# Kernel tuning notes

Measured on AMD Instinct MI355X. Metric: run time of the kernel, lower is better.

## Reference

```python
import jax, jax.numpy as jnp
import numpy as np
from jax import lax

B, S, H, V, J, K = 8, 512, 768, 35004, 30, 9
PAD = 0

def setup_inputs() -> dict:
    key = jax.random.key(0)
    ks = jax.random.split(key, 12)
    std = 0.02
    return {
        'x': jax.random.randint(ks[0], (B, S), 0, V),
        'decoder_input': jax.random.normal(ks[1], (B, J, H), jnp.float32),
        'encoder_output': jax.random.normal(ks[2], (B, S, H), jnp.float32),
        'hidden': jax.random.normal(ks[3], (1, B, H), jnp.float32),
        'teacher': jax.random.randint(ks[4], (B, J, K), 0, V),
        'max_len': K,
        'embed': jax.random.normal(ks[5], (V, H), jnp.float32) * std,
        'w_ih': jax.random.normal(ks[6], (3 * H, H), jnp.float32) * std,
        'w_hh': jax.random.normal(ks[7], (3 * H, H), jnp.float32) * std,
        'b_ih': jnp.zeros((3 * H,), jnp.float32),
        'b_hh': jnp.zeros((3 * H,), jnp.float32),
        'wg_w': jax.random.normal(ks[8], (1, 3 * H), jnp.float32) * std,
        'wg_b': jnp.zeros((1,), jnp.float32),
    }

def gru_cell(w, h, w_ih, w_hh, b_ih, b_hh):
    # PyTorch GRU gate order: reset, update, new
    gi = w @ w_ih.T + b_ih          # [B,3H]
    gh = h @ w_hh.T + b_hh          # [B,3H]
    ir, iz, inn = jnp.split(gi, 3, axis=-1)
    hr, hz, hn = jnp.split(gh, 3, axis=-1)
    r = jax.nn.sigmoid(ir + hr)
    z = jax.nn.sigmoid(iz + hz)
    n = jnp.tanh(inn + r * hn)
    return (1.0 - z) * n + z * h

def reference(x, decoder_input, encoder_output, hidden, teacher, max_len,
              embed, w_ih, w_hh, b_ih, b_hh, wg_w, wg_b):
    mask = (x == PAD)                      # [B,S]
    batch_ix = jnp.arange(x.shape[0])[:, None]

    def tok_step(carry, teach_t):
        w, h = carry                       # w,h: [B,H]; teach_t: [B]
        h = gru_cell(w, h, w_ih, w_hh, b_ih, b_hh)
        logits_hist = jnp.einsum('bsh,bh->bs', encoder_output, h)
        logits_hist = jnp.where(mask, -1e9, logits_hist)
        a_hist = jax.nn.softmax(logits_hist, axis=-1)          # [B,S]
        a_vocab = jax.nn.softmax(h @ embed.T, axis=-1)         # [B,V]
        context = jnp.einsum('bs,bsh->bh', a_hist, encoder_output)
        p_gen = jax.nn.sigmoid(
            jnp.concatenate([w, h, context], axis=-1) @ wg_w.T + wg_b)  # [B,1]
        p_ctx = jnp.zeros_like(a_vocab).at[batch_ix, x].add(a_hist)     # scatter_add pointer copy
        p_final = p_gen * a_vocab + (1.0 - p_gen) * p_ctx
        w_next = embed[teach_t]            # teacher forcing (dropout omitted: eval mode)
        return (w_next, h), p_final

    def slot_step(h, slot_in):
        w0, teach_j = slot_in              # w0: [B,H]; teach_j: [K,B]
        (_, h), p = lax.scan(tok_step, (w0, h), teach_j)
        return h, p                        # p: [K,B,V]

    h0 = hidden[0]                                      # [B,H]
    slots = jnp.swapaxes(decoder_input, 0, 1)           # [J,B,H]
    teach = jnp.transpose(teacher, (1, 2, 0))           # [J,K,B]
    _, outs = lax.scan(slot_step, h0, (slots, teach))   # [J,K,B,V]
    return jnp.transpose(outs, (2, 0, 1, 3))            # [B,J,K,V]
```

## Files before the change

### kernel.cpp

```cpp
#include <hip/hip_runtime.h>
#include <hip/hip_bf16.h>

typedef _Float16 f16;
typedef _Float16 f16x8 __attribute__((ext_vector_type(8)));
typedef _Float16 f16x4v __attribute__((ext_vector_type(4)));
typedef _Float16 h2 __attribute__((ext_vector_type(2)));
typedef float f32x4 __attribute__((ext_vector_type(4)));
typedef unsigned ui4v __attribute__((ext_vector_type(4)));
typedef unsigned long long ull;

#define B_ 8
#define S_ 512
#define H_ 768
#define V_ 35004
#define J_ 30
#define K_ 9
#define R_ 2160
#define H3 2304
#define VMT 17
#define VNT 274


__global__ void k_zero(int* p, int n) {
    int i = blockIdx.x * 256 + threadIdx.x;
    if (i < n) p[i] = 0;
}

__global__ void k_cast(const float* __restrict__ s, f16* __restrict__ d, long n) {
    for (long i = (long)blockIdx.x * 256 + threadIdx.x; i < n; i += (long)gridDim.x * 256)
        d[i] = (f16)s[i];
}

__global__ void k_build_wall(const float* __restrict__ emb, const float* __restrict__ dec,
                             const int* __restrict__ teacher, f16* __restrict__ Wall) {
    int r = blockIdx.x;
    int b = r / 270, s = r % 270, j = s / 9, t = s % 9;
    const float* src = (t == 0) ? dec + ((long)b * J_ + j) * H_
                                : emb + (long)teacher[((long)b * J_ + j) * K_ + (t - 1)] * H_;
    f16* dst = Wall + (long)r * H_;
    for (int c = threadIdx.x; c < H_; c += 256) dst[c] = (f16)src[c];
}

__global__ void k_init_h(const float* __restrict__ hidden, ull* __restrict__ hbuf) {
    int i = blockIdx.x * 256 + threadIdx.x;
    if (i < B_ * H_) {
        int b = i / H_, u = i % H_;
        hbuf[(long)b * 1536 + u] = (ull)__float_as_uint(hidden[i]);
    }
}

typedef const __attribute__((address_space(1))) unsigned GASU;
typedef __attribute__((address_space(3))) unsigned LASU;
__device__ __forceinline__ void gld16(const f16* g, f16* l) {
    __builtin_amdgcn_global_load_lds((GASU*)g, (LASU*)l, 16, 0, 0);
}

template <int MODE>
__global__ __launch_bounds__(256) void k_gemm(const f16* __restrict__ A, const f16* __restrict__ Bm,
                                              float* __restrict__ C, const float* __restrict__ bias,
                                              int M, int N, int K, long sA, long sB, long sC) {
    A += (long)blockIdx.z * sA;
    Bm += (long)blockIdx.z * sB;
    C += (long)blockIdx.z * sC;
    const int m0 = blockIdx.y * 128, n0 = blockIdx.x * 128;
    __shared__ f16 As[128 * 32];
    __shared__ f16 Bs[128 * 32];
    const int tid = threadIdx.x, lane = tid & 63, wave = tid >> 6;
    const int wm = wave >> 1, wn = wave & 1;
    const int fr = lane & 15, kg = lane >> 4;
    f32x4 acc[4][4] = {};
    const int idxu = wave * 128;
    const int i0 = idxu + lane, i1 = idxu + 64 + lane;
    const int r0 = i0 >> 2, k80 = i0 & 3;
    const int r1 = i1 >> 2, k81 = i1 & 3;
    int ga0 = m0 + r0; if (ga0 >= M) ga0 = M - 1;
    int ga1 = m0 + r1; if (ga1 >= M) ga1 = M - 1;
    int gb0 = n0 + r0; if (gb0 >= N) gb0 = N - 1;
    int gb1 = n0 + r1; if (gb1 >= N) gb1 = N - 1;
    const f16* pa0 = A + (long)ga0 * K + k80 * 8;
    const f16* pa1 = A + (long)ga1 * K + k81 * 8;
    const f16* pb0 = Bm + (long)gb0 * K + k80 * 8;
    const f16* pb1 = Bm + (long)gb1 * K + k81 * 8;
    for (int kt = 0; kt < K; kt += 32) {
        gld16(pa0 + kt, As + idxu * 8);
        gld16(pa1 + kt, As + idxu * 8 + 512);
        gld16(pb0 + kt, Bs + idxu * 8);
        gld16(pb1 + kt, Bs + idxu * 8 + 512);
        __syncthreads();
        f16x8 af[4], bf[4];
#pragma unroll
        for (int m = 0; m < 4; ++m) af[m] = *(const f16x8*)(As + (wm * 64 + m * 16 + fr) * 32 + kg * 8);
#pragma unroll
        for (int n = 0; n < 4; ++n) bf[n] = *(const f16x8*)(Bs + (wn * 64 + n * 16 + fr) * 32 + kg * 8);
#pragma unroll
        for (int m = 0; m < 4; ++m)
#pragma unroll
            for (int n = 0; n < 4; ++n)
                acc[m][n] = __builtin_amdgcn_mfma_f32_16x16x32_f16(af[m], bf[n], acc[m][n], 0, 0, 0);
        __syncthreads();
    }
    const int crow = m0 + wm * 64 + (lane >> 4) * 4;
    const int ccol = n0 + wn * 64 + fr;
#pragma unroll
    for (int n = 0; n < 4; ++n) {
        int col = ccol + n * 16;
        if (col >= N) continue;
        float bv = (MODE == 1) ? bias[col] : 0.f;
#pragma unroll
        for (int m = 0; m < 4; ++m) {
#pragma unroll
            for (int q = 0; q < 4; ++q) {
                int row = crow + m * 16 + q;
                if (row < M) C[(long)row * N + col] = acc[m][n][q] + bv;
            }
        }
    }
}

__global__ __launch_bounds__(256) void k_attn3(const f16* __restrict__ Ahi, const f16* __restrict__ Alo,
                                               const f16* __restrict__ Bhi, const f16* __restrict__ Blo,
                                               float* __restrict__ C, int M, int N, int K,
                                               long sA, long sB, long sC) {
    const long za = (long)blockIdx.z * sA, zb = (long)blockIdx.z * sB;
    C += (long)blockIdx.z * sC;
    const int m0 = blockIdx.y * 128, n0 = blockIdx.x * 128;
    __shared__ f16 As[128 * 32];
    __shared__ f16 Bs[128 * 32];
    const int tid = threadIdx.x, lane = tid & 63, wave = tid >> 6;
    const int wm = wave >> 1, wn = wave & 1;
    const int fr = lane & 15, kg = lane >> 4;
    f32x4 acc[4][4] = {};
    const int idxu = wave * 128;
    const int i0 = idxu + lane, i1 = idxu + 64 + lane;
    const int r0 = i0 >> 2, k80 = i0 & 3;
    const int r1 = i1 >> 2, k81 = i1 & 3;
    int ga0 = m0 + r0; if (ga0 >= M) ga0 = M - 1;
    int ga1 = m0 + r1; if (ga1 >= M) ga1 = M - 1;
    int gb0 = n0 + r0; if (gb0 >= N) gb0 = N - 1;
    int gb1 = n0 + r1; if (gb1 >= N) gb1 = N - 1;
    const long oa0 = (long)ga0 * K + k80 * 8, oa1 = (long)ga1 * K + k81 * 8;
    const long ob0 = (long)gb0 * K + k80 * 8, ob1 = (long)gb1 * K + k81 * 8;
    for (int ph = 0; ph < 3; ++ph) {
        const f16* Ap = (ph == 2 ? Alo : Ahi) + za;
        const f16* Bp = (ph == 1 ? Blo : Bhi) + zb;
        for (int kt = 0; kt < K; kt += 32) {
            gld16(Ap + oa0 + kt, As + idxu * 8);
            gld16(Ap + oa1 + kt, As + idxu * 8 + 512);
            gld16(Bp + ob0 + kt, Bs + idxu * 8);
            gld16(Bp + ob1 + kt, Bs + idxu * 8 + 512);
            __syncthreads();
            f16x8 af[4], bf[4];
#pragma unroll
            for (int m = 0; m < 4; ++m) af[m] = *(const f16x8*)(As + (wm * 64 + m * 16 + fr) * 32 + kg * 8);
#pragma unroll
            for (int n = 0; n < 4; ++n) bf[n] = *(const f16x8*)(Bs + (wn * 64 + n * 16 + fr) * 32 + kg * 8);
#pragma unroll
            for (int m = 0; m < 4; ++m)
#pragma unroll
                for (int n = 0; n < 4; ++n)
                    acc[m][n] = __builtin_amdgcn_mfma_f32_16x16x32_f16(af[m], bf[n], acc[m][n], 0, 0, 0);
            __syncthreads();
        }
    }
    const int crow = m0 + wm * 64 + (lane >> 4) * 4;
    const int ccol = n0 + wn * 64 + fr;
#pragma unroll
    for (int n = 0; n < 4; ++n) {
        int col = ccol + n * 16;
        if (col >= N) continue;
#pragma unroll
        for (int m = 0; m < 4; ++m) {
#pragma unroll
            for (int q = 0; q < 4; ++q) {
                int row = crow + m * 16 + q;
                if (row < M) C[(long)row * N + col] = acc[m][n][q];
            }
        }
    }
}

__global__ __launch_bounds__(256) void k_vocab(const f16* __restrict__ A, const f16* __restrict__ Bm,
                                               float* __restrict__ C, float* __restrict__ psum) {
    const int M = R_, N = V_, K = H_;
    const int nwg = VMT * VNT;
    int lin = blockIdx.x;
    int q8 = nwg / 8, r8 = nwg % 8;
    int xcd = lin & 7, idx = lin >> 3;
    int newlin = (xcd < r8) ? xcd * (q8 + 1) + idx : r8 * (q8 + 1) + (xcd - r8) * q8 + idx;
    int mt = newlin % VMT, nt = newlin / VMT;
    const int m0 = mt * 128, n0 = nt * 128;
    __shared__ f16 As[128 * 32];
    __shared__ f16 Bs[128 * 32];
    __shared__ float rpart[2][128];
    const int tid = threadIdx.x, lane = tid & 63, wave = tid >> 6;
    const int wm = wave >> 1, wn = wave & 1;
    const int fr = lane & 15, kg = lane >> 4;
    f32x4 acc[4][4] = {};
    const int idxu = wave * 128;
    const int i0 = idxu + lane, i1 = idxu + 64 + lane;
    const int r0 = i0 >> 2, k80 = i0 & 3;
    const int r1 = i1 >> 2, k81 = i1 & 3;
    int ga0 = m0 + r0; if (ga0 >= M) ga0 = M - 1;
    int ga1 = m0 + r1; if (ga1 >= M) ga1 = M - 1;
    int gb0 = n0 + r0; if (gb0 >= N) gb0 = N - 1;
    int gb1 = n0 + r1; if (gb1 >= N) gb1 = N - 1;
    const f16* pa0 = A + (long)ga0 * K + k80 * 8;
    const f16* pa1 = A + (long)ga1 * K + k81 * 8;
    const f16* pb0 = Bm + (long)gb0 * K + k80 * 8;
    const f16* pb1 = Bm + (long)gb1 * K + k81 * 8;
    for (int kt = 0; kt < K; kt += 32) {
        gld16(pa0 + kt, As + idxu * 8);
        gld16(pa1 + kt, As + idxu * 8 + 512);
        gld16(pb0 + kt, Bs + idxu * 8);
        gld16(pb1 + kt, Bs + idxu * 8 + 512);
        __syncthreads();
        f16x8 af[4], bf[4];
#pragma unroll
        for (int m = 0; m < 4; ++m) af[m] = *(const f16x8*)(As + (wm * 64 + m * 16 + fr) * 32 + kg * 8);
#pragma unroll
        for (int n = 0; n < 4; ++n) bf[n] = *(const f16x8*)(Bs + (wn * 64 + n * 16 + fr) * 32 + kg * 8);
#pragma unroll
        for (int m = 0; m < 4; ++m)
#pragma unroll
            for (int n = 0; n < 4; ++n)
                acc[m][n] = __builtin_amdgcn_mfma_f32_16x16x32_f16(af[m], bf[n], acc[m][n], 0, 0, 0);
        __syncthreads();
    }
    const int crow = m0 + wm * 64 + (lane >> 4) * 4;
    const int ccol = n0 + wn * 64 + fr;
    float rs[4][4];
#pragma unroll
    for (int m = 0; m < 4; ++m)
#pragma unroll
        for (int q = 0; q < 4; ++q) rs[m][q] = 0.f;
#pragma unroll
    for (int n = 0; n < 4; ++n) {
        int col = ccol + n * 16;
        if (col >= N) continue;
#pragma unroll
        for (int m = 0; m < 4; ++m) {
#pragma unroll
            for (int q = 0; q < 4; ++q) {
                int row = crow + m * 16 + q;
                if (row < M) {
                    float e = __expf(acc[m][n][q]);
                    C[(long)row * N + col] = e;
                    rs[m][q] += e;
                }
            }
        }
    }
#pragma unroll
    for (int m = 0; m < 4; ++m)
#pragma unroll
        for (int q = 0; q < 4; ++q) {
            float v = rs[m][q];
            v += __shfl_xor(v, 1);
            v += __shfl_xor(v, 2);
            v += __shfl_xor(v, 4);
            v += __shfl_xor(v, 8);
            rs[m][q] = v;
        }
    if ((lane & 15) == 0) {
#pragma unroll
        for (int m = 0; m < 4; ++m)
#pragma unroll
            for (int q = 0; q < 4; ++q)
                rpart[wn][wm * 64 + (lane >> 4) * 4 + m * 16 + q] = rs[m][q];
    }
    __syncthreads();
    if (tid < 128) {
        int row = m0 + tid;
        if (row < M) psum[(long)nt * M + row] = rpart[0][tid] + rpart[1][tid];
    }
}

__device__ __forceinline__ float fd2(unsigned hv, unsigned wv, float acc) {
#if __has_builtin(__builtin_amdgcn_fdot2)
    return __builtin_amdgcn_fdot2(__builtin_bit_cast(h2, hv), __builtin_bit_cast(h2, wv), acc, false);
#else
    h2 a = __builtin_bit_cast(h2, hv), b = __builtin_bit_cast(h2, wv);
    return acc + (float)a.x * (float)b.x + (float)a.y * (float)b.y;
#endif
}

__global__ __launch_bounds__(256, 1) void k_gru(const float* __restrict__ gi,
                                                const float* __restrict__ whh,
                                                const float* __restrict__ bhh,
                                                ull* hbuf,
                                                f16* __restrict__ Hhi, f16* __restrict__ Hlo,
                                                const float* __restrict__ emb, f16* __restrict__ emb16,
                                                const float* __restrict__ enc, f16* __restrict__ ehi,
                                                f16* __restrict__ elo, f16* __restrict__ encT) {
    __shared__ ui4v wsvu[9216];
    __shared__ __align__(16) f16 hsf[768];
    __shared__ float part[2][8][32][3];
    const int tid = threadIdx.x;
    if (blockIdx.x >= 192) {
        const long pt = (long)(blockIdx.x - 192) * 256 + tid;
        const long n4 = (long)V_ * H_ / 4;
        for (long i = pt; i < n4; i += 64 * 256) {
            f32x4 v = ((const f32x4*)emb)[i];
            f16x4v r = {(f16)v.x, (f16)v.y, (f16)v.z, (f16)v.w};
            ((f16x4v*)emb16)[i] = r;
        }
        const long n4e = (long)B_ * S_ * H_ / 4;
        for (long i = pt; i < n4e; i += 64 * 256) {
            f32x4 v = ((const f32x4*)enc)[i];
            long e0 = i * 4;
            int h = (int)(e0 % H_);
            long bs = e0 / H_;
            int ss = (int)(bs % S_), bb = (int)(bs / S_);
            f16 h0 = (f16)v.x, h1 = (f16)v.y, h2v = (f16)v.z, h3 = (f16)v.w;
            f16x4v hv = {h0, h1, h2v, h3};
            ((f16x4v*)ehi)[i] = hv;
            f16x4v lv = {(f16)(v.x - (float)h0), (f16)(v.y - (float)h1),
                         (f16)(v.z - (float)h2v), (f16)(v.w - (float)h3)};
            ((f16x4v*)elo)[i] = lv;
            f16* tp = encT + ((long)bb * H_ + h) * S_ + ss;
            tp[0] = h0;
            tp[S_] = h1;
            tp[2L * S_] = h2v;
            tp[3L * S_] = h3;
        }
        return;
    }
    const int chain = blockIdx.x / 24;
    const int blk = blockIdx.x % 24;
    const int u0 = blk * 32;
    for (int idx = tid; idx < 9216; idx += 256) {
        int uu = idx & 31, k8 = (idx >> 5) % 96, g = idx / (96 * 32);
        const float* src = whh + (long)(g * H_ + u0 + uu) * H_ + k8 * 8;
        f32x4 a = *(const f32x4*)src;
        f32x4 b2 = *(const f32x4*)(src + 4);
        f16x8 pk = {(f16)a.x, (f16)a.y, (f16)a.z, (f16)a.w,
                    (f16)b2.x, (f16)b2.y, (f16)b2.z, (f16)b2.w};
        wsvu[idx] = __builtin_bit_cast(ui4v, pk);
    }
    float b_r = 0.f, b_z = 0.f, b_n = 0.f;
    if (tid < 32) {
        int c = u0 + tid;
        b_r = bhh[c];
        b_z = bhh[H_ + c];
        b_n = bhh[2 * H_ + c];
    }
    __syncthreads();
    const int u = tid & 31, q = tid >> 5, lane = tid & 63;
    const int pw = (tid >> 6) * 192 + lane;
    ui4v wreg[3][12];
#pragma unroll
    for (int g = 0; g < 3; ++g)
#pragma unroll
        for (int i = 0; i < 12; ++i)
            wreg[g][i] = wsvu[(g * 96 + q * 12 + i) * 32 + u];
    ull* base = hbuf + (long)chain * 1536;
    const bool fin = (tid < 32);
    float g0 = 0.f, g1 = 0.f, g2v = 0.f;
    if (fin) {
        const float* gp = gi + (long)chain * 270 * H3;
        int c = u0 + tid;
        g0 = gp[c];
        g1 = gp[H_ + c];
        g2v = gp[2 * H_ + c];
    }
    for (int s = 0; s < 270; ++s) {
        const ull* rb = base + (s & 1) * 768;
        ull* wb = base + ((s + 1) & 1) * 768;
        const unsigned want = (unsigned)s;
        ull v0, v1, v2, vh = 0;
        for (;;) {
            v0 = __hip_atomic_load(rb + pw, __ATOMIC_RELAXED, __HIP_MEMORY_SCOPE_AGENT);
            v1 = __hip_atomic_load(rb + pw + 64, __ATOMIC_RELAXED, __HIP_MEMORY_SCOPE_AGENT);
            v2 = __hip_atomic_load(rb + pw + 128, __ATOMIC_RELAXED, __HIP_MEMORY_SCOPE_AGENT);
            bool ok = ((unsigned)(v0 >> 32) == want) & ((unsigned)(v1 >> 32) == want) &
                      ((unsigned)(v2 >> 32) == want);
            if (fin) {
                vh = __hip_atomic_load(rb + u0 + tid, __ATOMIC_RELAXED, __HIP_MEMORY_SCOPE_AGENT);
                ok &= ((unsigned)(vh >> 32) == want);
            }
            if (ok) break;
        }
        hsf[pw] = (f16)__uint_as_float((unsigned)v0);
        hsf[pw + 64] = (f16)__uint_as_float((unsigned)v1);
        hsf[pw + 128] = (f16)__uint_as_float((unsigned)v2);
        __builtin_amdgcn_wave_barrier();
        float ar = 0.f, az = 0.f, an = 0.f;
#pragma unroll
        for (int i = 0; i < 12; ++i) {
            ui4v hv = *(const ui4v*)(&hsf[(q * 12 + i) * 8]);
            ui4v wr = wreg[0][i], wz = wreg[1][i], wn = wreg[2][i];
            ar = fd2(hv.x, wr.x, ar); ar = fd2(hv.y, wr.y, ar);
            ar = fd2(hv.z, wr.z, ar); ar = fd2(hv.w, wr.w, ar);
            az = fd2(hv.x, wz.x, az); az = fd2(hv.y, wz.y, az);
            az = fd2(hv.z, wz.z, az); az = fd2(hv.w, wz.w, az);
            an = fd2(hv.x, wn.x, an); an = fd2(hv.y, wn.y, an);
            an = fd2(hv.z, wn.z, an); an = fd2(hv.w, wn.w, an);
        }
        const int par = s & 1;
        part[par][q][u][0] = ar;
        part[par][q][u][1] = az;
        part[par][q][u][2] = an;
        __syncthreads();
        if (fin) {
            float gr = b_r, gz = b_z, gn = b_n;
#pragma unroll
            for (int qq = 0; qq < 8; ++qq) {
                gr += part[par][qq][tid][0];
                gz += part[par][qq][tid][1];
                gn += part[par][qq][tid][2];
            }
            float hold = __uint_as_float((unsigned)vh);
            float rg = 1.f / (1.f + expf(-(g0 + gr)));
            float zg = 1.f / (1.f + expf(-(g1 + gz)));
            float ng = tanhf(g2v + rg * gn);
            float hnew = (1.f - zg) * ng + zg * hold;
            int c = u0 + tid;
            ull wvv = ((ull)(unsigned)(s + 1) << 32) | (ull)__float_as_uint(hnew);
            __hip_atomic_store(wb + c, wvv, __ATOMIC_RELAXED, __HIP_MEMORY_SCOPE_AGENT);
            long row = (long)chain * 270 + s;
            f16 h16 = (f16)hnew;
            Hhi[row * H_ + c] = h16;
            Hlo[row * H_ + c] = (f16)(hnew - (float)h16);
            if (s < 269) {
                const float* gp = gi + ((long)chain * 270 + s + 1) * H3;
                g0 = gp[c];
                g1 = gp[H_ + c];
                g2v = gp[2 * H_ + c];
            }
        }
    }
}

__global__ __launch_bounds__(256) void k_attn_softmax(const float* __restrict__ lg,
                                                      const int* __restrict__ x, f16* __restrict__ ah) {
    __shared__ float red[256];
    int r = blockIdx.x, tid = threadIdx.x;
    int b = r / 270;
    const float* lr = lg + (long)r * S_;
    const int* xb = x + (long)b * S_;
    float v0 = lr[tid];
    if (xb[tid] == 0) v0 = -1e9f;
    float v1 = lr[tid + 256];
    if (xb[tid + 256] == 0) v1 = -1e9f;
    red[tid] = fmaxf(v0, v1);
    __syncthreads();
    for (int o = 128; o > 0; o >>= 1) {
        if (tid < o) red[tid] = fmaxf(red[tid], red[tid + o]);
        __syncthreads();
    }
    float m = red[0];
    __syncthreads();
    float e0 = __expf(v0 - m), e1 = __expf(v1 - m);
    red[tid] = e0 + e1;
    __syncthreads();
    for (int o = 128; o > 0; o >>= 1) {
        if (tid < o) red[tid] += red[tid + o];
        __syncthreads();
    }
    float inv = 1.f / red[0];
    ah[(long)r * S_ + tid] = (f16)(e0 * inv);
    ah[(long)r * S_ + tid + 256] = (f16)(e1 * inv);
}

__global__ __launch_bounds__(256) void k_pgen(const f16* __restrict__ Wall, const f16* __restrict__ Hhi,
                                              const f16* __restrict__ Hlo, const float* __restrict__ ctx,
                                              const float* __restrict__ wg, const float* __restrict__ wgb,
                                              float* __restrict__ pg) {
    __shared__ float red[256];
    int r = blockIdx.x, tid = threadIdx.x;
    float a = 0.f;
    for (int i = tid; i < H_; i += 256) {
        a += (float)Wall[(long)r * H_ + i] * wg[i];
        a += ((float)Hhi[(long)r * H_ + i] + (float)Hlo[(long)r * H_ + i]) * wg[H_ + i];
        a += ctx[(long)r * H_ + i] * wg[2 * H_ + i];
    }
    red[tid] = a;
    __syncthreads();
    for (int o = 128; o > 0; o >>= 1) {
        if (tid < o) red[tid] += red[tid + o];
        __syncthreads();
    }
    if (tid == 0) pg[r] = 1.f / (1.f + expf(-(red[0] + wgb[0])));
}

__global__ void k_redsum(const float* __restrict__ psum, float* __restrict__ rinv, int nb) {
    int r = blockIdx.x * 256 + threadIdx.x;
    if (r >= R_) return;
    float s = 0.f;
    for (int b = 0; b < nb; ++b) s += psum[(long)b * R_ + r];
    rinv[r] = 1.f / s;
}

__global__ __launch_bounds__(256) void k_final(float* __restrict__ out, const float* __restrict__ rinv,
                                               const float* __restrict__ pg) {
    int r = blockIdx.y;
    int i = blockIdx.x * 256 + threadIdx.x;
    if (i >= V_ / 4) return;
    float scale = pg[r] * rinv[r];
    f32x4* po = (f32x4*)(out + (long)r * V_);
    f32x4 v = po[i];
    v.x *= scale;
    v.y *= scale;
    v.z *= scale;
    v.w *= scale;
    po[i] = v;
}

__global__ __launch_bounds__(512) void k_scatter(float* __restrict__ out, const f16* __restrict__ ah,
                                                 const float* __restrict__ pg, const int* __restrict__ x) {
    int r = blockIdx.x, s = threadIdx.x;
    int b = r / 270;
    int xv = x[(long)b * S_ + s];
    if (xv == 0) return;
    float a = (float)ah[(long)r * S_ + s];
    if (a == 0.f) return;
    atomicAdd(out + (long)r * V_ + xv, (1.f - pg[r]) * a);
}

extern "C" void kernel_launch(void* const* d_in, const int* in_sizes, int n_in, void* d_out,
                              int out_size, void* d_ws, size_t ws_size, hipStream_t stream) {
    (void)in_sizes; (void)n_in; (void)out_size; (void)ws_size;
    const int* x = (const int*)d_in[0];
    const float* dec = (const float*)d_in[1];
    const float* enc = (const float*)d_in[2];
    const float* hid = (const float*)d_in[3];
    const int* tea = (const int*)d_in[4];
    const float* emb = (const float*)d_in[6];
    const float* wih = (const float*)d_in[7];
    const float* whh = (const float*)d_in[8];
    const float* bih = (const float*)d_in[9];
    const float* bhh = (const float*)d_in[10];
    const float* wgw = (const float*)d_in[11];
    const float* wgb = (const float*)d_in[12];
    float* out = (float*)d_out;

    char* w = (char*)d_ws;
    size_t off = 0;
    auto alloc = [&](size_t bytes) {
        void* p = w + off;
        off = (off + bytes + 255) & ~(size_t)255;
        return p;
    };
    ull* hbuf = (ull*)alloc(8 * 1536 * 8);
    f16* Wall = (f16*)alloc((size_t)R_ * H_ * 2);
    f16* wih16 = (f16*)alloc((size_t)H3 * H_ * 2);
    float* giA = (float*)alloc((size_t)R_ * H3 * 4);
    f16* Hhi = (f16*)alloc((size_t)R_ * H_ * 2);
    f16* Hlo = (f16*)alloc((size_t)R_ * H_ * 2);
    f16* emb16 = (f16*)alloc((size_t)V_ * H_ * 2);
    f16* ehi = (f16*)alloc((size_t)B_ * S_ * H_ * 2);
    f16* elo = (f16*)alloc((size_t)B_ * S_ * H_ * 2);
    f16* encT = (f16*)alloc((size_t)B_ * H_ * S_ * 2);
    float* lgH = (float*)alloc((size_t)R_ * S_ * 4);
    f16* ah = (f16*)alloc((size_t)R_ * S_ * 2);
    float* ctx = (float*)alloc((size_t)R_ * H_ * 4);
    float* pg = (float*)alloc(R_ * 4);
    float* psum = (float*)alloc((size_t)VNT * R_ * 4);
    float* rinv = (float*)alloc(R_ * 4);

    const int nH = 8 * 1536 * 2;
    k_zero<<<(nH + 255) / 256, 256, 0, stream>>>((int*)hbuf, nH);
    k_cast<<<512, 256, 0, stream>>>(wih, wih16, (long)H3 * H_);
    k_build_wall<<<R_, 256, 0, stream>>>(emb, dec, tea, Wall);
    k_init_h<<<24, 256, 0, stream>>>(hid, hbuf);

    {
        dim3 g(H3 / 128, (R_ + 127) / 128, 1);
        k_gemm<1><<<g, 256, 0, stream>>>(Wall, wih16, giA, bih, R_, H3, H_, 0, 0, 0);
    }
    k_gru<<<256, 256, 0, stream>>>(giA, whh, bhh, hbuf, Hhi, Hlo,
                                   emb, emb16, enc, ehi, elo, encT);

    {
        dim3 g(S_ / 128, 3, 8);
        k_attn3<<<g, 256, 0, stream>>>(Hhi, Hlo, ehi, elo, lgH, 270, S_, H_,
                                       270L * H_, (long)S_ * H_, 270L * S_);
    }
    k_attn_softmax<<<R_, 256, 0, stream>>>(lgH, x, ah);
    {
        dim3 g(H_ / 128, 3, 8);
        k_gemm<0><<<g, 256, 0, stream>>>(ah, encT, ctx, nullptr, 270, H_, S_, 270L * S_, (long)H_ * S_, 270L * H_);
    }
    k_pgen<<<R_, 256, 0, stream>>>(Wall, Hhi, Hlo, ctx, wgw, wgb, pg);

    k_vocab<<<VMT * VNT, 256, 0, stream>>>(Hhi, emb16, out, psum);
    k_redsum<<<(R_ + 255) / 256, 256, 0, stream>>>(psum, rinv, VNT);
    {
        dim3 g((V_ / 4 + 255) / 256, R_, 1);
        k_final<<<g, 256, 0, stream>>>(out, rinv, pg);
    }
    k_scatter<<<R_, 512, 0, stream>>>(out, ah, pg, x);
}
```

Before: 1.121 ms.

## Store vocab exps as bf16 and fuse normalize+scatter in shared memory

The vocab GEMM now writes exp values as bf16 to a workspace buffer instead of fp32 into the output. A new per-row kernel reads them, scales them, applies the pointer scatter with shared-memory atomics, and writes the final row once, replacing the separate final-scale and global-atomic scatter kernels. The encoder transpose is also rewritten to write 8 contiguous f16 values per store instead of scattered single stores. bf16 rounding of the vocab probabilities reduces precision, and the new path needs extra workspace, falling back to the old path if it is too small.

```diff
diff --git a/kernel.cpp b/kernel.cpp
--- a/kernel.cpp
+++ b/kernel.cpp
@@ -7,6 +7,7 @@
 typedef _Float16 h2 __attribute__((ext_vector_type(2)));
 typedef float f32x4 __attribute__((ext_vector_type(4)));
 typedef unsigned ui4v __attribute__((ext_vector_type(4)));
+typedef unsigned short u16x4 __attribute__((ext_vector_type(4)));
 typedef unsigned long long ull;
 
 #define B_ 8
@@ -179,8 +180,10 @@
     }
 }
 
+template <int BF16OUT>
 __global__ __launch_bounds__(256) void k_vocab(const f16* __restrict__ A, const f16* __restrict__ Bm,
-                                               float* __restrict__ C, float* __restrict__ psum) {
+                                               float* __restrict__ Cf, unsigned short* __restrict__ Ch,
+                                               float* __restrict__ psum) {
     const int M = R_, N = V_, K = H_;
     const int nwg = VMT * VNT;
     int lin = blockIdx.x;
@@ -244,7 +247,13 @@
                 int row = crow + m * 16 + q;
                 if (row < M) {
                     float e = __expf(acc[m][n][q]);
-                    C[(long)row * N + col] = e;
+                    if (BF16OUT) {
+                        unsigned u = __float_as_uint(e);
+                        u += 0x7FFFu + ((u >> 16) & 1u);
+                        Ch[(long)row * N + col] = (unsigned short)(u >> 16);
+                    } else {
+                        Cf[(long)row * N + col] = e;
+                    }
                     rs[m][q] += e;
                 }
             }
@@ -307,21 +316,23 @@
         const long n4e = (long)B_ * S_ * H_ / 4;
         for (long i = pt; i < n4e; i += 64 * 256) {
             f32x4 v = ((const f32x4*)enc)[i];
-            long e0 = i * 4;
-            int h = (int)(e0 % H_);
-            long bs = e0 / H_;
-            int ss = (int)(bs % S_), bb = (int)(bs / S_);
             f16 h0 = (f16)v.x, h1 = (f16)v.y, h2v = (f16)v.z, h3 = (f16)v.w;
             f16x4v hv = {h0, h1, h2v, h3};
             ((f16x4v*)ehi)[i] = hv;
             f16x4v lv = {(f16)(v.x - (float)h0), (f16)(v.y - (float)h1),
                          (f16)(v.z - (float)h2v), (f16)(v.w - (float)h3)};
             ((f16x4v*)elo)[i] = lv;
-            f16* tp = encT + ((long)bb * H_ + h) * S_ + ss;
-            tp[0] = h0;
-            tp[S_] = h1;
-            tp[2L * S_] = h2v;
-            tp[3L * S_] = h3;
+        }
+        const long nOct = 8L * 768 * 64;
+        for (long o = pt; o < nOct; o += 64 * 256) {
+            int s8 = (int)(o & 63);
+            int h = (int)((o >> 6) % 768);
+            int bb = (int)(o / (64 * 768));
+            const float* sp = enc + ((long)bb * S_ + s8 * 8) * H_ + h;
+            f16x8 r;
+#pragma unroll
+            for (int i = 0; i < 8; ++i) r[i] = (f16)sp[(long)i * H_];
+            *(f16x8*)(encT + ((long)bb * H_ + h) * S_ + s8 * 8) = r;
         }
         return;
     }
@@ -491,6 +502,42 @@
     rinv[r] = 1.f / s;
 }
 
+__global__ __launch_bounds__(256, 1) void k_fin2(const unsigned short* __restrict__ expv,
+                                                 const float* __restrict__ rinv,
+                                                 const float* __restrict__ pg,
+                                                 const f16* __restrict__ ah,
+                                                 const int* __restrict__ x,
+                                                 float* __restrict__ out) {
+    __shared__ float row[V_];
+    const int r = blockIdx.x, tid = threadIdx.x;
+    const int b = r / 270;
+    const float pgv = pg[r];
+    const float scale = pgv * rinv[r];
+    const unsigned short* ep = expv + (long)r * V_;
+    for (int i = tid; i < V_ / 4; i += 256) {
+        u16x4 v = ((const u16x4*)ep)[i];
+        f32x4 o;
+        o.x = __uint_as_float((unsigned)v.x << 16) * scale;
+        o.y = __uint_as_float((unsigned)v.y << 16) * scale;
+        o.z = __uint_as_float((unsigned)v.z << 16) * scale;
+        o.w = __uint_as_float((unsigned)v.w << 16) * scale;
+        ((f32x4*)row)[i] = o;
+    }
+    __syncthreads();
+    const float om = 1.f - pgv;
+    for (int s = tid; s < S_; s += 256) {
+        int xv = x[(long)b * S_ + s];
+        if (xv != 0) {
+            float a = (float)ah[(long)r * S_ + s];
+            if (a != 0.f) atomicAdd(&row[xv], om * a);
+        }
+    }
+    __syncthreads();
+    float* orow = out + (long)r * V_;
+    for (int i = tid; i < V_ / 4; i += 256)
+        ((f32x4*)orow)[i] = ((const f32x4*)row)[i];
+}
+
 __global__ __launch_bounds__(256) void k_final(float* __restrict__ out, const float* __restrict__ rinv,
                                                const float* __restrict__ pg) {
     int r = blockIdx.y;
@@ -519,7 +566,7 @@
 
 extern "C" void kernel_launch(void* const* d_in, const int* in_sizes, int n_in, void* d_out,
                               int out_size, void* d_ws, size_t ws_size, hipStream_t stream) {
-    (void)in_sizes; (void)n_in; (void)out_size; (void)ws_size;
+    (void)in_sizes; (void)n_in; (void)out_size;
     const int* x = (const int*)d_in[0];
     const float* dec = (const float*)d_in[1];
     const float* enc = (const float*)d_in[2];
@@ -557,6 +604,8 @@
     float* pg = (float*)alloc(R_ * 4);
     float* psum = (float*)alloc((size_t)VNT * R_ * 4);
     float* rinv = (float*)alloc(R_ * 4);
+    unsigned short* expv = (unsigned short*)alloc((size_t)R_ * V_ * 2);
+    const bool fused = (off <= ws_size);
 
     const int nH = 8 * 1536 * 2;
     k_zero<<<(nH + 255) / 256, 256, 0, stream>>>((int*)hbuf, nH);
@@ -583,11 +632,15 @@
     }
     k_pgen<<<R_, 256, 0, stream>>>(Wall, Hhi, Hlo, ctx, wgw, wgb, pg);
 
-    k_vocab<<<VMT * VNT, 256, 0, stream>>>(Hhi, emb16, out, psum);
-    k_redsum<<<(R_ + 255) / 256, 256, 0, stream>>>(psum, rinv, VNT);
-    {
+    if (fused) {
+        k_vocab<1><<<VMT * VNT, 256, 0, stream>>>(Hhi, emb16, nullptr, expv, psum);
+        k_redsum<<<(R_ + 255) / 256, 256, 0, stream>>>(psum, rinv, VNT);
+        k_fin2<<<R_, 256, 0, stream>>>(expv, rinv, pg, ah, x, out);
+    } else {
+        k_vocab<0><<<VMT * VNT, 256, 0, stream>>>(Hhi, emb16, out, nullptr, psum);
+        k_redsum<<<(R_ + 255) / 256, 256, 0, stream>>>(psum, rinv, VNT);
         dim3 g((V_ / 4 + 255) / 256, R_, 1);
         k_final<<<g, 256, 0, stream>>>(out, rinv, pg);
-    }
-    k_scatter<<<R_, 512, 0, stream>>>(out, ah, pg, x);
-}
+        k_scatter<<<R_, 512, 0, stream>>>(out, ah, pg, x);
+    }
+}
```

Result: no change. 1.134 ms (+1.2%).

## Fuse row-sum, scale and pointer scatter into one kernel; tile encoder transpose

Applied to the files above, without the earlier changes.

Replaces the separate row-sum, scale and global-atomic scatter kernels with one kernel per output row. It reduces the partial sums, scales the row while staging it in LDS, applies the pointer-copy atomics in LDS, and writes the row back once. This removes one extra full read and write pass of the large output and the global atomics. Separately, the encoder transpose to fp16 now goes through a padded 64x64 LDS tile instead of strided scalar global stores. The fused kernel uses about 140KB of LDS per block, so only one block fits per CU, which may limit latency hiding.

```diff
diff --git a/kernel.cpp b/kernel.cpp
--- a/kernel.cpp
+++ b/kernel.cpp
@@ -307,21 +307,30 @@
         const long n4e = (long)B_ * S_ * H_ / 4;
         for (long i = pt; i < n4e; i += 64 * 256) {
             f32x4 v = ((const f32x4*)enc)[i];
-            long e0 = i * 4;
-            int h = (int)(e0 % H_);
-            long bs = e0 / H_;
-            int ss = (int)(bs % S_), bb = (int)(bs / S_);
             f16 h0 = (f16)v.x, h1 = (f16)v.y, h2v = (f16)v.z, h3 = (f16)v.w;
             f16x4v hv = {h0, h1, h2v, h3};
             ((f16x4v*)ehi)[i] = hv;
             f16x4v lv = {(f16)(v.x - (float)h0), (f16)(v.y - (float)h1),
                          (f16)(v.z - (float)h2v), (f16)(v.w - (float)h3)};
             ((f16x4v*)elo)[i] = lv;
-            f16* tp = encT + ((long)bb * H_ + h) * S_ + ss;
-            tp[0] = h0;
-            tp[S_] = h1;
-            tp[2L * S_] = h2v;
-            tp[3L * S_] = h3;
+        }
+        float* tl = (float*)wsvu;
+        for (int t = blockIdx.x - 192; t < 8 * 8 * 12; t += 64) {
+            int ht = t % 12, st = (t / 12) % 8, bb = t / 96;
+            __syncthreads();
+#pragma unroll
+            for (int k = 0; k < 16; ++k) {
+                int i = tid + k * 256;
+                int sl = i >> 6, hl = i & 63;
+                tl[sl * 65 + hl] = enc[((long)bb * S_ + st * 64 + sl) * H_ + ht * 64 + hl];
+            }
+            __syncthreads();
+#pragma unroll
+            for (int k = 0; k < 16; ++k) {
+                int i = tid + k * 256;
+                int hl = i >> 6, sl = i & 63;
+                encT[((long)bb * H_ + ht * 64 + hl) * S_ + st * 64 + sl] = (f16)tl[sl * 65 + hl];
+            }
         }
         return;
     }
@@ -483,38 +492,46 @@
     if (tid == 0) pg[r] = 1.f / (1.f + expf(-(red[0] + wgb[0])));
 }
 
-__global__ void k_redsum(const float* __restrict__ psum, float* __restrict__ rinv, int nb) {
-    int r = blockIdx.x * 256 + threadIdx.x;
-    if (r >= R_) return;
+__global__ __launch_bounds__(256, 1) void k_fin3(float* __restrict__ out,
+                                                 const float* __restrict__ psum,
+                                                 const float* __restrict__ pg,
+                                                 const f16* __restrict__ ah,
+                                                 const int* __restrict__ x) {
+    __shared__ float row[V_];
+    __shared__ float red[256];
+    const int r = blockIdx.x, tid = threadIdx.x;
+    const int b = r / 270;
     float s = 0.f;
-    for (int b = 0; b < nb; ++b) s += psum[(long)b * R_ + r];
-    rinv[r] = 1.f / s;
-}
-
-__global__ __launch_bounds__(256) void k_final(float* __restrict__ out, const float* __restrict__ rinv,
-                                               const float* __restrict__ pg) {
-    int r = blockIdx.y;
-    int i = blockIdx.x * 256 + threadIdx.x;
-    if (i >= V_ / 4) return;
-    float scale = pg[r] * rinv[r];
-    f32x4* po = (f32x4*)(out + (long)r * V_);
-    f32x4 v = po[i];
-    v.x *= scale;
-    v.y *= scale;
-    v.z *= scale;
-    v.w *= scale;
-    po[i] = v;
-}
-
-__global__ __launch_bounds__(512) void k_scatter(float* __restrict__ out, const f16* __restrict__ ah,
-                                                 const float* __restrict__ pg, const int* __restrict__ x) {
-    int r = blockIdx.x, s = threadIdx.x;
-    int b = r / 270;
-    int xv = x[(long)b * S_ + s];
-    if (xv == 0) return;
-    float a = (float)ah[(long)r * S_ + s];
-    if (a == 0.f) return;
-    atomicAdd(out + (long)r * V_ + xv, (1.f - pg[r]) * a);
+    for (int i = tid; i < VNT; i += 256) s += psum[(long)i * R_ + r];
+    red[tid] = s;
+    __syncthreads();
+    for (int o = 128; o > 0; o >>= 1) {
+        if (tid < o) red[tid] += red[tid + o];
+        __syncthreads();
+    }
+    const float pgv = pg[r];
+    const float scale = pgv / red[0];
+    float* orow = out + (long)r * V_;
+    for (int i = tid; i < V_ / 4; i += 256) {
+        f32x4 v = ((const f32x4*)orow)[i];
+        v.x *= scale;
+        v.y *= scale;
+        v.z *= scale;
+        v.w *= scale;
+        ((f32x4*)row)[i] = v;
+    }
+    __syncthreads();
+    const float om = 1.f - pgv;
+    for (int s2 = tid; s2 < S_; s2 += 256) {
+        int xv = x[(long)b * S_ + s2];
+        if (xv != 0) {
+            float a = (float)ah[(long)r * S_ + s2];
+            if (a != 0.f) atomicAdd(&row[xv], om * a);
+        }
+    }
+    __syncthreads();
+    for (int i = tid; i < V_ / 4; i += 256)
+        ((f32x4*)orow)[i] = ((const f32x4*)row)[i];
 }
 
 extern "C" void kernel_launch(void* const* d_in, const int* in_sizes, int n_in, void* d_out,
@@ -556,7 +573,6 @@
     float* ctx = (float*)alloc((size_t)R_ * H_ * 4);
     float* pg = (float*)alloc(R_ * 4);
     float* psum = (float*)alloc((size_t)VNT * R_ * 4);
-    float* rinv = (float*)alloc(R_ * 4);
 
     const int nH = 8 * 1536 * 2;
     k_zero<<<(nH + 255) / 256, 256, 0, stream>>>((int*)hbuf, nH);
@@ -584,10 +600,5 @@
     k_pgen<<<R_, 256, 0, stream>>>(Wall, Hhi, Hlo, ctx, wgw, wgb, pg);
 
     k_vocab<<<VMT * VNT, 256, 0, stream>>>(Hhi, emb16, out, psum);
-    k_redsum<<<(R_ + 255) / 256, 256, 0, stream>>>(psum, rinv, VNT);
-    {
-        dim3 g((V_ / 4 + 255) / 256, R_, 1);
-        k_final<<<g, 256, 0, stream>>>(out, rinv, pg);
-    }
-    k_scatter<<<R_, 512, 0, stream>>>(out, ah, pg, x);
-}
+    k_fin3<<<R_, 256, 0, stream>>>(out, psum, pg, ah, x);
+}
```

After: 1.117 ms. No clear change (-0.3%).
